# Kernel tuning notes

Measured on AMD Instinct MI355X. Metric: run time of the kernel, lower is better.

## Reference

```python
import jax, jax.numpy as jnp
import numpy as np

S = 16          # spatial_size (adaptive pool output per dim)
EPS = 1e-8      # torch.cosine_similarity eps

def _avg_pool3d(x, s):
    # exact adaptive avg pool when D,H,W divisible by s
    B, C, D, H, W = x.shape
    kd, kh, kw = D // s, H // s, W // s
    x = x.reshape(B, C, s, kd, s, kh, s, kw)
    return x.mean(axis=(3, 5, 7))  # (B, C, s, s, s)

def _flatten_rows(x):
    # (B,C,s,s,s) -> (B*s^3, C), matching view+transpose+flatten
    B, C = x.shape[0], x.shape[1]
    return x.reshape(B, C, -1).transpose(0, 2, 1).reshape(-1, C)

def _cos_sim_matrix(a):
    # pairwise cosine similarity via normalize + GEMM
    norms = jnp.maximum(jnp.linalg.norm(a, axis=-1, keepdims=True), EPS)
    an = a / norms
    return an @ an.T  # (N, N)

def setup_inputs() -> dict:
    key = jax.random.key(0)
    k1, k2 = jax.random.split(key)
    shape = (2, 32, 64, 64, 64)
    p1 = jax.random.normal(k1, shape, dtype=jnp.float32)
    p2 = jax.random.normal(k2, shape, dtype=jnp.float32)
    return {"p1": p1, "p2": p2}

def reference(p1, p2):
    aa = _flatten_rows(_avg_pool3d(p1, S))  # (N, C), N = B*S^3
    bb = _flatten_rows(_avg_pool3d(p2, S))
    sim_a = _cos_sim_matrix(aa)
    sim_b = _cos_sim_matrix(bb)
    return jnp.mean((sim_a - sim_b) ** 2)  # MSELoss
```

## Files before the change

kernel.cpp:

```cpp
#include <hip/hip_runtime.h>
#include <hip/hip_bf16.h>


#define HW    4096
#define DHW   262144
#define NROW  8192
#define C     32
#define NPART 16

__global__ __launch_bounds__(1024) void fused_pool_gram_kernel(
    const float* __restrict__ p1, const float* __restrict__ p2,
    float* __restrict__ G)
{
    const int bid = blockIdx.x;
    const int yo = bid & 15;
    const int zo = (bid >> 4) & 15;
    const int b  = bid >> 8;

    const int tid  = threadIdx.x;
    const int wv   = tid >> 6;
    const int lane = tid & 63;
    const int dy   = lane >> 4;
    const int x4   = lane & 15;

    __shared__ float pa[C][17];
    __shared__ float pb[C][17];
    __shared__ float inva[16];
    __shared__ float invb[16];

    const size_t sp_off = (size_t)(4 * zo) * HW + (size_t)(4 * yo + dy) * 64 + 4 * x4;

    float4 va[2][4], vb[2][4];
    #pragma unroll
    for (int cc = 0; cc < 2; ++cc) {
        const int c = wv * 2 + cc;
        const float* basea = p1 + (size_t)(b * C + c) * DHW + sp_off;
        const float* baseb = p2 + (size_t)(b * C + c) * DHW + sp_off;
        #pragma unroll
        for (int dz = 0; dz < 4; ++dz) {
            va[cc][dz] = *reinterpret_cast<const float4*>(basea + dz * HW);
            vb[cc][dz] = *reinterpret_cast<const float4*>(baseb + dz * HW);
        }
    }
    __builtin_amdgcn_sched_barrier(0);

    #pragma unroll
    for (int cc = 0; cc < 2; ++cc) {
        float sa = 0.f, sb = 0.f;
        #pragma unroll
        for (int dz = 0; dz < 4; ++dz) {
            sa += (va[cc][dz].x + va[cc][dz].y) + (va[cc][dz].z + va[cc][dz].w);
            sb += (vb[cc][dz].x + vb[cc][dz].y) + (vb[cc][dz].z + vb[cc][dz].w);
        }
        sa += __shfl_xor(sa, 16);  sa += __shfl_xor(sa, 32);
        sb += __shfl_xor(sb, 16);  sb += __shfl_xor(sb, 32);
        if (lane < 16) {
            pa[wv * 2 + cc][lane] = sa * (1.0f / 64.0f);
            pb[wv * 2 + cc][lane] = sb * (1.0f / 64.0f);
        }
    }
    __syncthreads();

    if (tid < 32) {
        const int x = tid & 15;
        float ss = 0.f;
        if (tid < 16) {
            #pragma unroll
            for (int c2 = 0; c2 < C; ++c2) { const float v = pa[c2][x]; ss += v * v; }
            inva[x] = 1.0f / fmaxf(sqrtf(ss), 1e-8f);
        } else {
            #pragma unroll
            for (int c2 = 0; c2 < C; ++c2) { const float v = pb[c2][x]; ss += v * v; }
            invb[x] = 1.0f / fmaxf(sqrtf(ss), 1e-8f);
        }
    }
    __syncthreads();

    {
        const int sel = tid >> 9;
        const int c   = (tid >> 4) & 31;
        const int x   = tid & 15;
        if (sel == 0) pa[c][x] *= inva[x];
        else          pb[c][x] *= invb[x];
    }
    __syncthreads();

    const int k = tid >> 5;
    const int l = tid & 31;
    float gaa = 0.f, gab = 0.f, gbb = 0.f;
    #pragma unroll
    for (int x = 0; x < 16; ++x) {
        const float ak = pa[k][x];
        const float al = pa[l][x];
        const float bk = pb[k][x];
        const float bl = pb[l][x];
        gaa += ak * al;
        gab += ak * bl;
        gbb += bk * bl;
    }

    float* Gp = G + (size_t)(bid & (NPART - 1)) * 3072;
    atomicAdd(&Gp[       k * 32 + l], gaa);
    atomicAdd(&Gp[1024 + k * 32 + l], gab);
    atomicAdd(&Gp[2048 + k * 32 + l], gbb);
}

__global__ __launch_bounds__(1024) void finalize_kernel(
    const float* __restrict__ G, float* __restrict__ out)
{
    const int t = threadIdx.x;
    float gaa = 0.f, gab = 0.f, gbb = 0.f;
    #pragma unroll
    for (int p = 0; p < NPART; ++p) {
        gaa += G[p * 3072 + t];
        gab += G[p * 3072 + 1024 + t];
        gbb += G[p * 3072 + 2048 + t];
    }
    float v = gaa * gaa + gbb * gbb - 2.f * gab * gab;

    __shared__ float red[16];
    #pragma unroll
    for (int off = 32; off > 0; off >>= 1) v += __shfl_down(v, off);
    if ((t & 63) == 0) red[t >> 6] = v;
    __syncthreads();
    if (t < 16) {
        float w = red[t];
        #pragma unroll
        for (int off = 8; off > 0; off >>= 1) w += __shfl_down(w, off);
        if (t == 0) out[0] = w / ((float)NROW * (float)NROW);
    }
}

extern "C" void kernel_launch(void* const* d_in, const int* in_sizes, int n_in,
                              void* d_out, int out_size, void* d_ws, size_t ws_size,
                              hipStream_t stream) {
    const float* p1 = (const float*)d_in[0];
    const float* p2 = (const float*)d_in[1];
    float* out = (float*)d_out;

    float* G = (float*)d_ws;

    hipMemsetAsync(G, 0, NPART * 3072 * sizeof(float), stream);

    fused_pool_gram_kernel<<<512, 1024, 0, stream>>>(p1, p2, G);
    finalize_kernel<<<1, 1024, 0, stream>>>(G, out);
}
```

Baseline: 151.3 us.

## Fuse finalize into main kernel using last-block-done atomic counter

Removes the separate finalize launch: each block increments a global counter after its Gram atomics, and the last block to arrive reduces the partial Gram matrices and writes the loss. It also cuts the number of partial Gram copies from 16 to 4 and drops the sched_barrier after the loads. Fewer partial copies means more atomic contention per address, and the counter adds a fence per block in exchange for saving one kernel launch.

Measured after the change: 177.5 us. 1.17x slower.

```diff
diff --git a/kernel.cpp b/kernel.cpp
--- a/kernel.cpp
+++ b/kernel.cpp
@@ -1,16 +1,18 @@
 #include <hip/hip_runtime.h>
-#include <hip/hip_bf16.h>
 
 
 #define HW    4096
 #define DHW   262144
 #define NROW  8192
 #define C     32
-#define NPART 16
+#define NPART 4
+#define NBLK  512
 
-__global__ __launch_bounds__(1024) void fused_pool_gram_kernel(
+__global__ __launch_bounds__(1024) void fused_region_loss_kernel(
     const float* __restrict__ p1, const float* __restrict__ p2,
-    float* __restrict__ G)
+    float* __restrict__ G,
+    unsigned* __restrict__ cnt,
+    float* __restrict__ out)
 {
     const int bid = blockIdx.x;
     const int yo = bid & 15;
@@ -42,7 +44,6 @@
             vb[cc][dz] = *reinterpret_cast<const float4*>(baseb + dz * HW);
         }
     }
-    __builtin_amdgcn_sched_barrier(0);
 
     #pragma unroll
     for (int cc = 0; cc < 2; ++cc) {
@@ -100,34 +101,45 @@
     }
 
     float* Gp = G + (size_t)(bid & (NPART - 1)) * 3072;
-    atomicAdd(&Gp[       k * 32 + l], gaa);
-    atomicAdd(&Gp[1024 + k * 32 + l], gab);
-    atomicAdd(&Gp[2048 + k * 32 + l], gbb);
-}
+    atomicAdd(&Gp[       tid], gaa);
+    atomicAdd(&Gp[1024 + tid], gab);
+    atomicAdd(&Gp[2048 + tid], gbb);
 
-__global__ __launch_bounds__(1024) void finalize_kernel(
-    const float* __restrict__ G, float* __restrict__ out)
-{
-    const int t = threadIdx.x;
-    float gaa = 0.f, gab = 0.f, gbb = 0.f;
-    #pragma unroll
-    for (int p = 0; p < NPART; ++p) {
-        gaa += G[p * 3072 + t];
-        gab += G[p * 3072 + 1024 + t];
-        gbb += G[p * 3072 + 2048 + t];
+    __syncthreads();
+    __shared__ unsigned my_order;
+    if (tid == 0) {
+        __threadfence();
+        my_order = __hip_atomic_fetch_add(cnt, 1u, __ATOMIC_ACQ_REL,
+                                          __HIP_MEMORY_SCOPE_AGENT);
     }
-    float v = gaa * gaa + gbb * gbb - 2.f * gab * gab;
+    __syncthreads();
+    if (my_order != NBLK - 1) return;
 
-    __shared__ float red[16];
-    #pragma unroll
-    for (int off = 32; off > 0; off >>= 1) v += __shfl_down(v, off);
-    if ((t & 63) == 0) red[t >> 6] = v;
-    __syncthreads();
-    if (t < 16) {
-        float w = red[t];
+    __threadfence();
+    {
+        float s0 = 0.f, s1 = 0.f, s2 = 0.f;
         #pragma unroll
-        for (int off = 8; off > 0; off >>= 1) w += __shfl_down(w, off);
-        if (t == 0) out[0] = w / ((float)NROW * (float)NROW);
+        for (int p = 0; p < NPART; ++p) {
+            s0 += __hip_atomic_load(&G[p * 3072 +        tid], __ATOMIC_RELAXED,
+                                    __HIP_MEMORY_SCOPE_AGENT);
+            s1 += __hip_atomic_load(&G[p * 3072 + 1024 + tid], __ATOMIC_RELAXED,
+                                    __HIP_MEMORY_SCOPE_AGENT);
+            s2 += __hip_atomic_load(&G[p * 3072 + 2048 + tid], __ATOMIC_RELAXED,
+                                    __HIP_MEMORY_SCOPE_AGENT);
+        }
+        float v = s0 * s0 + s2 * s2 - 2.f * s1 * s1;
+
+        __shared__ float red[16];
+        #pragma unroll
+        for (int off = 32; off > 0; off >>= 1) v += __shfl_down(v, off);
+        if ((tid & 63) == 0) red[tid >> 6] = v;
+        __syncthreads();
+        if (tid < 16) {
+            float w = red[tid];
+            #pragma unroll
+            for (int off = 8; off > 0; off >>= 1) w += __shfl_down(w, off);
+            if (tid == 0) out[0] = w / ((float)NROW * (float)NROW);
+        }
     }
 }
 
@@ -138,10 +150,10 @@
     const float* p2 = (const float*)d_in[1];
     float* out = (float*)d_out;
 
-    float* G = (float*)d_ws;
+    float* G      = (float*)d_ws;
+    unsigned* cnt = (unsigned*)((char*)d_ws + NPART * 3072 * sizeof(float));
 
-    hipMemsetAsync(G, 0, NPART * 3072 * sizeof(float), stream);
+    hipMemsetAsync(d_ws, 0, NPART * 3072 * sizeof(float) + 64, stream);
 
-    fused_pool_gram_kernel<<<512, 1024, 0, stream>>>(p1, p2, G);
-    finalize_kernel<<<1, 1024, 0, stream>>>(G, out);
+    fused_region_loss_kernel<<<NBLK, 1024, 0, stream>>>(p1, p2, G, cnt, out);
 }
```
